# Kernel optimization log

Measured on AMD Instinct MI355X. Metric: run time of the kernel, lower is better.

## Reference

```python
import jax, jax.numpy as jnp
import numpy as np

EPS = 1e-5
NUM_GROUPS = 16


def _deform_conv(x, offset, mask, weight):
    """Modulated deformable conv v2, 3x3, stride 1, pad 1, no bias.
    x: [B,C,H,W], offset: [B,18,H,W] (y,x interleaved per kernel point),
    mask: [B,9,H,W], weight: [O,C,3,3].
    """
    B, C, H, W = x.shape
    O = weight.shape[0]
    K = 9
    off = offset.reshape(B, K, 2, H, W)
    dy, dx = off[:, :, 0], off[:, :, 1]  # [B,K,H,W]
    # base sampling grid: output pixel + kernel tap offset (pad=1 -> taps -1..1)
    ky, kx = jnp.meshgrid(jnp.arange(3), jnp.arange(3), indexing='ij')
    ky = (ky.reshape(K) - 1).astype(x.dtype)
    kx = (kx.reshape(K) - 1).astype(x.dtype)
    iy = jnp.arange(H, dtype=x.dtype)[:, None]
    ix = jnp.arange(W, dtype=x.dtype)[None, :]
    py = iy[None, None] + ky[None, :, None, None] + dy  # [B,K,H,W]
    px = ix[None, None] + kx[None, :, None, None] + dx

    y0 = jnp.floor(py)
    x0 = jnp.floor(px)
    wy = py - y0  # grad flows to offsets via these weights
    wx = px - x0

    xf = x.reshape(B, C, H * W)

    def gather(yc, xc, w):
        # yc,xc,w: [B,K,H,W] float; returns weighted samples [B,C,K,H,W]
        valid = (yc >= 0) & (yc <= H - 1) & (xc >= 0) & (xc <= W - 1)
        yi = jnp.clip(yc, 0, H - 1).astype(jnp.int32)
        xi = jnp.clip(xc, 0, W - 1).astype(jnp.int32)
        idx = (yi * W + xi).reshape(B, K * H * W)
        g = jax.vmap(lambda xb, ib: xb[:, ib])(xf, idx)  # [B,C,K*H*W]
        g = g.reshape(B, C, K, H, W)
        wv = (w * valid.astype(x.dtype))[:, None]  # [B,1,K,H,W]
        return g * wv

    val = gather(y0, x0, (1 - wy) * (1 - wx))
    val = val + gather(y0, x0 + 1, (1 - wy) * wx)
    val = val + gather(y0 + 1, x0, wy * (1 - wx))
    val = val + gather(y0 + 1, x0 + 1, wy * wx)

    val = val * mask[:, None]  # modulation: [B,C,K,H,W] * [B,1,K,H,W]
    w = weight.reshape(O, C, K)
    return jnp.einsum('bckhw,ock->bohw', val, w)


def _group_norm(y, gamma, beta):
    B, O, H, W = y.shape
    g = y.reshape(B, NUM_GROUPS, O // NUM_GROUPS, H, W)
    mean = g.mean(axis=(2, 3, 4), keepdims=True)
    var = ((g - mean) ** 2).mean(axis=(2, 3, 4), keepdims=True)
    g = (g - mean) * jax.lax.rsqrt(var + EPS)
    y = g.reshape(B, O, H, W)
    return y * gamma[None, :, None, None] + beta[None, :, None, None]


def setup_inputs() -> dict:
    key = jax.random.key(0)
    k1, k2, k3, k4 = jax.random.split(key, 4)
    B, C, O, H, W = 8, 256, 256, 64, 64
    x = jax.random.normal(k1, (B, C, H, W), jnp.float32)
    offset = jax.random.normal(k2, (B, 18, H, W), jnp.float32)
    mask = jax.random.uniform(k3, (B, 9, H, W), jnp.float32)
    weight = jax.random.normal(k4, (O, C, 3, 3), jnp.float32) * 0.02
    gamma = jnp.ones((O,), jnp.float32)
    beta = jnp.zeros((O,), jnp.float32)
    return {"x": x, "offset": offset, "mask": mask, "weight": weight,
            "gamma": gamma, "beta": beta}


def reference(x, offset, mask, weight, gamma, beta):
    y = _deform_conv(x, offset, mask, weight)
    return _group_norm(y, gamma, beta)
```

## Files before the change

kernel.cpp:

```cpp
#include <hip/hip_runtime.h>
#include <hip/hip_fp16.h>
#include <math.h>

#define BB 8
#define CC 256
#define OO 256
#define HH 64
#define WW 64
#define KK 9
#define HWSZ 4096
#define CKSZ 2304
#define NG 16
#define OPG 16
#define EPSV 1e-5f

typedef _Float16 f16;
typedef f16 f16x8 __attribute__((ext_vector_type(8)));
typedef float f32x4 __attribute__((ext_vector_type(4)));

#define XH_ELEMS ((size_t)BB*HWSZ*CC)
#define WH_ELEMS ((size_t)OO*CKSZ)
#define CV_ELEMS ((size_t)BB*OO*HWSZ)
#define PSUM_FLOATS ((size_t)512*32)

__device__ __forceinline__ void gload_lds16(const void* g, void* l) {
  __builtin_amdgcn_global_load_lds(
      (const __attribute__((address_space(1))) void*)g,
      (__attribute__((address_space(3))) void*)l, 16, 0, 0);
}

__global__ __launch_bounds__(256) void x_transpose_k(
    const float* __restrict__ x, __half* __restrict__ xh)
{
  int blk = blockIdx.x;
  int b = blk >> 8; int rem = blk & 255;
  int c0 = (rem >> 6) * 64; int hw0 = (rem & 63) * 64;
  __shared__ float st[64][65];
  int t = threadIdx.x;
  #pragma unroll
  for (int i = 0; i < 16; ++i) {
    int idx = t + i*256; int c = idx >> 6, w = idx & 63;
    st[c][w] = x[((size_t)(b*CC + c0 + c))*HWSZ + hw0 + w];
  }
  __syncthreads();
  #pragma unroll
  for (int i = 0; i < 8; ++i) {
    int idx = t + i*256; int r = idx >> 5, cp = idx & 31;
    __half2 v = __floats2half2_rn(st[cp*2][r], st[cp*2+1][r]);
    *(__half2*)&xh[((size_t)(b*HWSZ) + hw0 + r)*CC + c0 + cp*2] = v;
  }
}

__global__ __launch_bounds__(256) void w_reorder_k(
    const float* __restrict__ w, __half* __restrict__ wh)
{
  int i = blockIdx.x*256 + threadIdx.x;
  int o = i / CKSZ; int kp = i - o*CKSZ;
  int kk = kp >> 8, c = kp & 255;
  wh[i] = __float2half(w[o*CKSZ + c*KK + kk]);
}

template<int F16OUT>
__global__ __launch_bounds__(256, 2) void dcn_mfma_k(
    const float* __restrict__ off, const float* __restrict__ msk,
    const __half* __restrict__ xh, const __half* __restrict__ wh,
    float* __restrict__ out32, __half* __restrict__ conv16,
    float* __restrict__ psum)
{
  __shared__ __half sWl[OO*64];
  __shared__ __half sVl[2][64*64];
  __shared__ uint   sTapO[KK][64][4];
  __shared__ __half sTapW[KK][64][4];
  __shared__ float  sRed[4][4][2];

  const int t = threadIdx.x;
  const int b = blockIdx.x & 7;
  const int h = blockIdx.x >> 3;

  const int lane = t & 63, wid = t >> 6;
  const int lr = lane & 15, lh = lane >> 4;
  const int gp = t >> 2, gq = t & 3;

  for (int s = t; s < KK*64; s += 256) {
    int k = s >> 6, p = s & 63;
    float dy = off[(((b*18) + 2*k    )*HH + h)*WW + p];
    float dx = off[(((b*18) + 2*k + 1)*HH + h)*WW + p];
    float m  = msk[(((b*KK) + k)*HH + h)*WW + p];
    float py = (float)(h + (k/3) - 1) + dy;
    float px = (float)(p + (k%3) - 1) + dx;
    float y0f = floorf(py), x0f = floorf(px);
    float wy = py - y0f, wx = px - x0f;
    int y0 = (int)y0f, x0 = (int)x0f;
    #pragma unroll
    for (int tap = 0; tap < 4; ++tap) {
      int yy = y0 + (tap >> 1), xx = x0 + (tap & 1);
      bool v = (yy >= 0) & (yy < HH) & (xx >= 0) & (xx < WW);
      float bw = ((tap >> 1) ? wy : 1.f - wy) * ((tap & 1) ? wx : 1.f - wx);
      float wgt = v ? bw * m : 0.f;
      int cy = min(max(yy, 0), HH-1), cx = min(max(xx, 0), WW-1);
      sTapO[k][p][tap] = (uint)((cy*WW + cx) * (CC*2));
      sTapW[k][p][tap] = __float2half(wgt);
    }
  }
  __syncthreads();

  f32x4 acc[4][4];
  #pragma unroll
  for (int mi = 0; mi < 4; ++mi)
    #pragma unroll
    for (int ni = 0; ni < 4; ++ni) acc[mi][ni] = (f32x4){0.f,0.f,0.f,0.f};

  const char* xbase = (const char*)xh + (size_t)b * (HWSZ*CC*2);

  uint4 tO = *(const uint4*)&sTapO[0][gp][0];
  union { uint2 u; __half hh[4]; } tW;
  tW.u = *(const uint2*)&sTapW[0][gp][0];

  auto gload_sw = [&](int k, int c0) {
    #pragma unroll
    for (int i = 0; i < 8; ++i) {
      int idx = i*256 + t;
      int o = idx >> 3, s = idx & 7;
      const __half* g = wh + (size_t)o*CKSZ + k*256 + c0 + ((s ^ (o & 7)) << 3);
      char* ldsbase = (char*)sWl + (size_t)(i*256 + (t & ~63))*16;
      gload_lds16(g, ldsbase);
    }
  };

  gload_sw(0, 0);
  {
    __half2 w0 = __half2half2(tW.hh[0]), w1 = __half2half2(tW.hh[1]);
    __half2 w2 = __half2half2(tW.hh[2]), w3 = __half2half2(tW.hh[3]);
    #pragma unroll
    for (int oi = 0; oi < 2; ++oi) {
      int oct = gq + oi*4;
      const char* cb = xbase + oct*16;
      uint4 r0 = *(const uint4*)(cb + tO.x);
      uint4 r1 = *(const uint4*)(cb + tO.y);
      uint4 r2 = *(const uint4*)(cb + tO.z);
      uint4 r3 = *(const uint4*)(cb + tO.w);
      const __half2* t0 = (const __half2*)&r0; const __half2* t1 = (const __half2*)&r1;
      const __half2* t2 = (const __half2*)&r2; const __half2* t3 = (const __half2*)&r3;
      __half2 o_[4];
      #pragma unroll
      for (int r = 0; r < 4; ++r)
        o_[r] = __hfma2(w0, t0[r], __hfma2(w1, t1[r],
                __hfma2(w2, t2[r], __hmul2(w3, t3[r]))));
      *(uint4*)&sVl[0][gp*64 + ((oct ^ (gp & 7)) << 3)] = *(uint4*)o_;
    }
  }

  int cur = 0;
  for (int cc = 0; cc < 36; ++cc) {
    const int k = cc >> 2;
    __syncthreads();

    f16x8 areg[2][4];
    #pragma unroll
    for (int ks = 0; ks < 2; ++ks)
      #pragma unroll
      for (int mi = 0; mi < 4; ++mi) {
        int r = wid*64 + mi*16 + lr;
        areg[ks][mi] = *(const f16x8*)&sWl[r*64 + (((ks*4 + lh) ^ (r & 7)) << 3)];
      }
    __syncthreads();

    uint4 ga0, ga1, ga2, ga3, gb0, gb1, gb2, gb3;
    bool pf = (cc + 1 < 36);
    int kn = (cc+1) >> 2, c0n = ((cc+1) & 3) << 6;
    if (pf) {
      gload_sw(kn, c0n);
      if (kn != k) {
        tO = *(const uint4*)&sTapO[kn][gp][0];
        tW.u = *(const uint2*)&sTapW[kn][gp][0];
      }
      const char* cb = xbase + (size_t)(c0n*2) + gq*16;
      ga0 = *(const uint4*)(cb + tO.x);
      ga1 = *(const uint4*)(cb + tO.y);
      ga2 = *(const uint4*)(cb + tO.z);
      ga3 = *(const uint4*)(cb + tO.w);
      gb0 = *(const uint4*)(cb + tO.x + 64);
      gb1 = *(const uint4*)(cb + tO.y + 64);
      gb2 = *(const uint4*)(cb + tO.z + 64);
      gb3 = *(const uint4*)(cb + tO.w + 64);
    }

    #pragma unroll
    for (int ks = 0; ks < 2; ++ks) {
      f16x8 brg[4];
      #pragma unroll
      for (int ni = 0; ni < 4; ++ni) {
        int r = ni*16 + lr;
        brg[ni] = *(const f16x8*)&sVl[cur][r*64 + (((ks*4 + lh) ^ (r & 7)) << 3)];
      }
      #pragma unroll
      for (int mi = 0; mi < 4; ++mi)
        #pragma unroll
        for (int ni = 0; ni < 4; ++ni)
          acc[mi][ni] = __builtin_amdgcn_mfma_f32_16x16x32_f16(
              areg[ks][mi], brg[ni], acc[mi][ni], 0, 0, 0);
    }

    if (pf) {
      __half2 w0 = __half2half2(tW.hh[0]), w1 = __half2half2(tW.hh[1]);
      __half2 w2 = __half2half2(tW.hh[2]), w3 = __half2half2(tW.hh[3]);
      {
        const __half2* t0 = (const __half2*)&ga0; const __half2* t1 = (const __half2*)&ga1;
        const __half2* t2 = (const __half2*)&ga2; const __half2* t3 = (const __half2*)&ga3;
        __half2 o_[4];
        #pragma unroll
        for (int r = 0; r < 4; ++r)
          o_[r] = __hfma2(w0, t0[r], __hfma2(w1, t1[r],
                  __hfma2(w2, t2[r], __hmul2(w3, t3[r]))));
        *(uint4*)&sVl[cur ^ 1][gp*64 + ((gq ^ (gp & 7)) << 3)] = *(uint4*)o_;
      }
      {
        const __half2* t0 = (const __half2*)&gb0; const __half2* t1 = (const __half2*)&gb1;
        const __half2* t2 = (const __half2*)&gb2; const __half2* t3 = (const __half2*)&gb3;
        __half2 o_[4];
        #pragma unroll
        for (int r = 0; r < 4; ++r)
          o_[r] = __hfma2(w0, t0[r], __hfma2(w1, t1[r],
                  __hfma2(w2, t2[r], __hmul2(w3, t3[r]))));
        *(uint4*)&sVl[cur ^ 1][gp*64 + (((gq + 4) ^ (gp & 7)) << 3)] = *(uint4*)o_;
      }
      cur ^= 1;
    }
  }

  #pragma unroll
  for (int mi = 0; mi < 4; ++mi) {
    #pragma unroll
    for (int ni = 0; ni < 4; ++ni) {
      int ob = wid*64 + mi*16 + lh*4;
      int pp = ni*16 + lr;
      #pragma unroll
      for (int j = 0; j < 4; ++j) {
        size_t idx = ((size_t)(b*OO + ob + j))*HWSZ + h*WW + pp;
        if (F16OUT) conv16[idx] = __float2half(acc[mi][ni][j]);
        else        out32[idx] = acc[mi][ni][j];
      }
    }
  }

  if (F16OUT) {
    #pragma unroll
    for (int mi = 0; mi < 4; ++mi) {
      float s1 = 0.f, s2 = 0.f;
      #pragma unroll
      for (int ni = 0; ni < 4; ++ni)
        #pragma unroll
        for (int j = 0; j < 4; ++j) {
          float v = acc[mi][ni][j];
          s1 += v; s2 += v*v;
        }
      #pragma unroll
      for (int d = 32; d > 0; d >>= 1) {
        s1 += __shfl_xor(s1, d);
        s2 += __shfl_xor(s2, d);
      }
      if (lane == 0) { sRed[wid][mi][0] = s1; sRed[wid][mi][1] = s2; }
    }
    __syncthreads();
    if (t < 16) {
      psum[(size_t)blockIdx.x*32 + t*2]     = sRed[t >> 2][t & 3][0];
      psum[(size_t)blockIdx.x*32 + t*2 + 1] = sRed[t >> 2][t & 3][1];
    }
  }
}

__global__ __launch_bounds__(256) void gn_norm2_k(
    const __half* __restrict__ conv16, const float* __restrict__ psum,
    const float* __restrict__ gamma, const float* __restrict__ beta,
    float* __restrict__ out)
{
  int bid = blockIdx.x;
  int bo = bid >> 1;
  int b = bo >> 8, o = bo & 255;
  int g = o >> 4;
  float s1 = 0.f, s2 = 0.f;
  for (int hbl = 0; hbl < 64; ++hbl) {
    s1 += psum[(size_t)(hbl*8 + b)*32 + g*2];
    s2 += psum[(size_t)(hbl*8 + b)*32 + g*2 + 1];
  }
  const float invN = 1.f / (float)(OPG*HWSZ);
  float mean = s1 * invN;
  float var  = s2 * invN - mean*mean;
  float inv = rsqrtf(var + EPSV);
  float sc = gamma[o]*inv;
  float sh = beta[o] - mean*sc;

  size_t e0 = ((size_t)(b*OO + o))*HWSZ + (size_t)(bid & 1)*2048
            + (size_t)threadIdx.x*8;
  uint4 u = *(const uint4*)(conv16 + e0);
  const __half2* hh = (const __half2*)&u;
  float r[8];
  #pragma unroll
  for (int j = 0; j < 4; ++j) {
    float2 f = __half22float2(hh[j]);
    r[2*j] = f.x; r[2*j+1] = f.y;
  }
  *(float4*)&out[e0]     = make_float4(r[0]*sc+sh, r[1]*sc+sh, r[2]*sc+sh, r[3]*sc+sh);
  *(float4*)&out[e0 + 4] = make_float4(r[4]*sc+sh, r[5]*sc+sh, r[6]*sc+sh, r[7]*sc+sh);
}

__global__ __launch_bounds__(1024) void gn_stats_k(
    const float* __restrict__ out, float* __restrict__ stats)
{
  int bg = blockIdx.x;
  const float4* p = (const float4*)(out + (size_t)bg*OPG*HWSZ);
  const int n4 = OPG*HWSZ/4;
  float s1 = 0.f, s2 = 0.f;
  for (int i = threadIdx.x; i < n4; i += 1024) {
    float4 v = p[i];
    s1 += v.x + v.y + v.z + v.w;
    s2 += v.x*v.x + v.y*v.y + v.z*v.z + v.w*v.w;
  }
  #pragma unroll
  for (int o2 = 32; o2 > 0; o2 >>= 1) {
    s1 += __shfl_down(s1, o2);
    s2 += __shfl_down(s2, o2);
  }
  __shared__ float r1[16], r2[16];
  int wd = threadIdx.x >> 6, lane = threadIdx.x & 63;
  if (lane == 0) { r1[wd] = s1; r2[wd] = s2; }
  __syncthreads();
  if (threadIdx.x == 0) {
    float t1 = 0.f, t2 = 0.f;
    #pragma unroll
    for (int i = 0; i < 16; i++) { t1 += r1[i]; t2 += r2[i]; }
    const float invN = 1.f / (float)(OPG*HWSZ);
    float mean = t1 * invN;
    float var  = t2 * invN - mean*mean;
    stats[bg*2]   = mean;
    stats[bg*2+1] = var;
  }
}

__global__ __launch_bounds__(256) void gn_norm_k(
    float* __restrict__ out, const float* __restrict__ stats,
    const float* __restrict__ gamma, const float* __restrict__ beta)
{
  size_t i = (size_t)blockIdx.x*256 + threadIdx.x;
  const size_t n4 = (size_t)BB*OO*HWSZ/4;
  if (i >= n4) return;
  size_t base = i*4;
  int bo = (int)(base / HWSZ);
  int b = bo / OO, o = bo - b*OO;
  int g = o >> 4;
  float mean = stats[(b*NG+g)*2], var = stats[(b*NG+g)*2+1];
  float inv = rsqrtf(var + EPSV);
  float sc = gamma[o]*inv;
  float sh = beta[o] - mean*sc;
  float4 v = *(float4*)&out[base];
  v.x = v.x*sc + sh; v.y = v.y*sc + sh;
  v.z = v.z*sc + sh; v.w = v.w*sc + sh;
  *(float4*)&out[base] = v;
}

extern "C" void kernel_launch(void* const* d_in, const int* in_sizes, int n_in,
                              void* d_out, int out_size, void* d_ws, size_t ws_size,
                              hipStream_t stream) {
  const float* x      = (const float*)d_in[0];
  const float* offset = (const float*)d_in[1];
  const float* mask   = (const float*)d_in[2];
  const float* weight = (const float*)d_in[3];
  const float* gamma  = (const float*)d_in[4];
  const float* beta   = (const float*)d_in[5];
  float* out = (float*)d_out;

  __half* xh   = (__half*)d_ws;
  __half* wh   = xh + XH_ELEMS;
  __half* cv   = wh + WH_ELEMS;
  float* psum  = (float*)(cv + CV_ELEMS);

  const size_t need = (XH_ELEMS + WH_ELEMS + CV_ELEMS)*2 + PSUM_FLOATS*4 + 1024;

  x_transpose_k<<<BB*4*64, 256, 0, stream>>>(x, xh);
  w_reorder_k<<<(int)(WH_ELEMS/256), 256, 0, stream>>>(weight, wh);

  if (ws_size >= need) {
    dcn_mfma_k<1><<<512, 256, 0, stream>>>(offset, mask, xh, wh,
                                           (float*)nullptr, cv, psum);
    gn_norm2_k<<<4096, 256, 0, stream>>>(cv, psum, gamma, beta, out);
  } else {
    float* stats = (float*)(wh + WH_ELEMS);
    dcn_mfma_k<0><<<512, 256, 0, stream>>>(offset, mask, xh, wh,
                                           out, (__half*)nullptr, (float*)nullptr);
    gn_stats_k<<<BB*NG, 1024, 0, stream>>>(out, stats);
    gn_norm_k<<<(int)((size_t)BB*OO*HWSZ/4 + 255)/256, 256, 0, stream>>>(
        out, stats, gamma, beta);
  }
}
```

Baseline: 93.41 us.

## Pre-swizzle weights into MFMA fragment order and load A operands directly from global

The weight reorder kernel now writes fp16 weights in the exact per-lane MFMA A-fragment order, so the main kernel loads A registers straight from global memory (coalesced 16-byte loads) instead of staging a 32KB weight tile through LDS. This removes the LDS weight buffer, one of the two barriers per iteration, and the async global-to-LDS copies. Tap offsets and weights are packed into one 32-bit word per tap, and launch bounds go up to 3 blocks per CU to use the freed LDS. The trade-off is that each wave reloads weight fragments from L2/global every iteration, adding latency that LDS staging used to hide.

```diff
diff --git a/kernel.cpp b/kernel.cpp
--- a/kernel.cpp
+++ b/kernel.cpp
@@ -19,15 +19,9 @@
 typedef float f32x4 __attribute__((ext_vector_type(4)));
 
 #define XH_ELEMS ((size_t)BB*HWSZ*CC)
-#define WH_ELEMS ((size_t)OO*CKSZ)
+#define WF_ELEMS ((size_t)OO*CKSZ)
 #define CV_ELEMS ((size_t)BB*OO*HWSZ)
 #define PSUM_FLOATS ((size_t)512*32)
-
-__device__ __forceinline__ void gload_lds16(const void* g, void* l) {
-  __builtin_amdgcn_global_load_lds(
-      (const __attribute__((address_space(1))) void*)g,
-      (__attribute__((address_space(3))) void*)l, 16, 0, 0);
-}
 
 __global__ __launch_bounds__(256) void x_transpose_k(
     const float* __restrict__ x, __half* __restrict__ xh)
@@ -51,26 +45,27 @@
   }
 }
 
-__global__ __launch_bounds__(256) void w_reorder_k(
-    const float* __restrict__ w, __half* __restrict__ wh)
+__global__ __launch_bounds__(256) void w_frag_k(
+    const float* __restrict__ w, __half* __restrict__ wf)
 {
   int i = blockIdx.x*256 + threadIdx.x;
-  int o = i / CKSZ; int kp = i - o*CKSZ;
-  int kk = kp >> 8, c = kp & 255;
-  wh[i] = __float2half(w[o*CKSZ + c*KK + kk]);
+  int e = i & 7, lane = (i >> 3) & 63, mi = (i >> 9) & 3;
+  int ks = (i >> 11) & 1, wid = (i >> 12) & 3, cc = i >> 14;
+  int k = cc >> 2, c0i = cc & 3;
+  int o = wid*64 + mi*16 + (lane & 15);
+  int c = c0i*64 + ks*32 + (lane >> 4)*8 + e;
+  wf[i] = __float2half(w[(o*CC + c)*KK + k]);
 }
 
 template<int F16OUT>
-__global__ __launch_bounds__(256, 2) void dcn_mfma_k(
+__global__ __launch_bounds__(256, 3) void dcn_mfma_k(
     const float* __restrict__ off, const float* __restrict__ msk,
-    const __half* __restrict__ xh, const __half* __restrict__ wh,
+    const __half* __restrict__ xh, const __half* __restrict__ wf,
     float* __restrict__ out32, __half* __restrict__ conv16,
     float* __restrict__ psum)
 {
-  __shared__ __half sWl[OO*64];
   __shared__ __half sVl[2][64*64];
-  __shared__ uint   sTapO[KK][64][4];
-  __shared__ __half sTapW[KK][64][4];
+  __shared__ uint   sTapP[KK][64][4];
   __shared__ float  sRed[4][4][2];
 
   const int t = threadIdx.x;
@@ -98,8 +93,9 @@
       float bw = ((tap >> 1) ? wy : 1.f - wy) * ((tap & 1) ? wx : 1.f - wx);
       float wgt = v ? bw * m : 0.f;
       int cy = min(max(yy, 0), HH-1), cx = min(max(xx, 0), WW-1);
-      sTapO[k][p][tap] = (uint)((cy*WW + cx) * (CC*2));
-      sTapW[k][p][tap] = __float2half(wgt);
+      uint idx = (uint)(cy*WW + cx);
+      sTapP[k][p][tap] = (idx << 16)
+                       | (uint)__half_as_ushort(__float2half(wgt));
     }
   }
   __syncthreads();
@@ -112,77 +108,75 @@
 
   const char* xbase = (const char*)xh + (size_t)b * (HWSZ*CC*2);
 
-  uint4 tO = *(const uint4*)&sTapO[0][gp][0];
-  union { uint2 u; __half hh[4]; } tW;
-  tW.u = *(const uint2*)&sTapW[0][gp][0];
-
-  auto gload_sw = [&](int k, int c0) {
-    #pragma unroll
-    for (int i = 0; i < 8; ++i) {
-      int idx = i*256 + t;
-      int o = idx >> 3, s = idx & 7;
-      const __half* g = wh + (size_t)o*CKSZ + k*256 + c0 + ((s ^ (o & 7)) << 3);
-      char* ldsbase = (char*)sWl + (size_t)(i*256 + (t & ~63))*16;
-      gload_lds16(g, ldsbase);
-    }
+  uint toff[4]; __half2 twv[4];
+  #pragma unroll
+  for (int i = 0; i < 4; ++i) {
+    uint tp = sTapP[0][gp][i];
+    toff[i] = (tp >> 16) << 9;
+    twv[i]  = __half2half2(__ushort_as_half((unsigned short)(tp & 0xFFFFu)));
+  }
+  int tk = 0;
+
+  auto combine_write = [&](uint4 r0, uint4 r1, uint4 r2, uint4 r3,
+                           int oct, __half* dst) {
+    const __half2* t0 = (const __half2*)&r0; const __half2* t1 = (const __half2*)&r1;
+    const __half2* t2 = (const __half2*)&r2; const __half2* t3 = (const __half2*)&r3;
+    __half2 o_[4];
+    #pragma unroll
+    for (int r = 0; r < 4; ++r)
+      o_[r] = __hfma2(twv[0], t0[r], __hfma2(twv[1], t1[r],
+              __hfma2(twv[2], t2[r], __hmul2(twv[3], t3[r]))));
+    *(uint4*)&dst[gp*64 + ((oct ^ (gp & 7)) << 3)] = *(uint4*)o_;
   };
 
-  gload_sw(0, 0);
   {
-    __half2 w0 = __half2half2(tW.hh[0]), w1 = __half2half2(tW.hh[1]);
-    __half2 w2 = __half2half2(tW.hh[2]), w3 = __half2half2(tW.hh[3]);
-    #pragma unroll
-    for (int oi = 0; oi < 2; ++oi) {
-      int oct = gq + oi*4;
-      const char* cb = xbase + oct*16;
-      uint4 r0 = *(const uint4*)(cb + tO.x);
-      uint4 r1 = *(const uint4*)(cb + tO.y);
-      uint4 r2 = *(const uint4*)(cb + tO.z);
-      uint4 r3 = *(const uint4*)(cb + tO.w);
-      const __half2* t0 = (const __half2*)&r0; const __half2* t1 = (const __half2*)&r1;
-      const __half2* t2 = (const __half2*)&r2; const __half2* t3 = (const __half2*)&r3;
-      __half2 o_[4];
-      #pragma unroll
-      for (int r = 0; r < 4; ++r)
-        o_[r] = __hfma2(w0, t0[r], __hfma2(w1, t1[r],
-                __hfma2(w2, t2[r], __hmul2(w3, t3[r]))));
-      *(uint4*)&sVl[0][gp*64 + ((oct ^ (gp & 7)) << 3)] = *(uint4*)o_;
-    }
+    const char* cb = xbase + gq*16;
+    uint4 a0 = *(const uint4*)(cb + toff[0]);
+    uint4 a1 = *(const uint4*)(cb + toff[1]);
+    uint4 a2 = *(const uint4*)(cb + toff[2]);
+    uint4 a3 = *(const uint4*)(cb + toff[3]);
+    uint4 b0 = *(const uint4*)(cb + toff[0] + 64);
+    uint4 b1 = *(const uint4*)(cb + toff[1] + 64);
+    uint4 b2 = *(const uint4*)(cb + toff[2] + 64);
+    uint4 b3 = *(const uint4*)(cb + toff[3] + 64);
+    combine_write(a0, a1, a2, a3, gq,     sVl[0]);
+    combine_write(b0, b1, b2, b3, gq + 4, sVl[0]);
   }
 
   int cur = 0;
   for (int cc = 0; cc < 36; ++cc) {
-    const int k = cc >> 2;
     __syncthreads();
 
+    const __half* wfp = wf + (size_t)(cc*4 + wid)*4096 + lane*8;
     f16x8 areg[2][4];
     #pragma unroll
     for (int ks = 0; ks < 2; ++ks)
       #pragma unroll
-      for (int mi = 0; mi < 4; ++mi) {
-        int r = wid*64 + mi*16 + lr;
-        areg[ks][mi] = *(const f16x8*)&sWl[r*64 + (((ks*4 + lh) ^ (r & 7)) << 3)];
-      }
-    __syncthreads();
-
-    uint4 ga0, ga1, ga2, ga3, gb0, gb1, gb2, gb3;
+      for (int mi = 0; mi < 4; ++mi)
+        areg[ks][mi] = *(const f16x8*)(wfp + (ks*4 + mi)*512);
+
     bool pf = (cc + 1 < 36);
     int kn = (cc+1) >> 2, c0n = ((cc+1) & 3) << 6;
+    uint4 ga0, ga1, ga2, ga3, gb0, gb1, gb2, gb3;
     if (pf) {
-      gload_sw(kn, c0n);
-      if (kn != k) {
-        tO = *(const uint4*)&sTapO[kn][gp][0];
-        tW.u = *(const uint2*)&sTapW[kn][gp][0];
+      if (kn != tk) {
+        #pragma unroll
+        for (int i = 0; i < 4; ++i) {
+          uint tp = sTapP[kn][gp][i];
+          toff[i] = (tp >> 16) << 9;
+          twv[i]  = __half2half2(__ushort_as_half((unsigned short)(tp & 0xFFFFu)));
+        }
+        tk = kn;
       }
       const char* cb = xbase + (size_t)(c0n*2) + gq*16;
-      ga0 = *(const uint4*)(cb + tO.x);
-      ga1 = *(const uint4*)(cb + tO.y);
-      ga2 = *(const uint4*)(cb + tO.z);
-      ga3 = *(const uint4*)(cb + tO.w);
-      gb0 = *(const uint4*)(cb + tO.x + 64);
-      gb1 = *(const uint4*)(cb + tO.y + 64);
-      gb2 = *(const uint4*)(cb + tO.z + 64);
-      gb3 = *(const uint4*)(cb + tO.w + 64);
+      ga0 = *(const uint4*)(cb + toff[0]);
+      ga1 = *(const uint4*)(cb + toff[1]);
+      ga2 = *(const uint4*)(cb + toff[2]);
+      ga3 = *(const uint4*)(cb + toff[3]);
+      gb0 = *(const uint4*)(cb + toff[0] + 64);
+      gb1 = *(const uint4*)(cb + toff[1] + 64);
+      gb2 = *(const uint4*)(cb + toff[2] + 64);
+      gb3 = *(const uint4*)(cb + toff[3] + 64);
     }
 
     #pragma unroll
@@ -202,28 +196,8 @@
     }
 
     if (pf) {
-      __half2 w0 = __half2half2(tW.hh[0]), w1 = __half2half2(tW.hh[1]);
-      __half2 w2 = __half2half2(tW.hh[2]), w3 = __half2half2(tW.hh[3]);
-      {
-        const __half2* t0 = (const __half2*)&ga0; const __half2* t1 = (const __half2*)&ga1;
-        const __half2* t2 = (const __half2*)&ga2; const __half2* t3 = (const __half2*)&ga3;
-        __half2 o_[4];
-        #pragma unroll
-        for (int r = 0; r < 4; ++r)
-          o_[r] = __hfma2(w0, t0[r], __hfma2(w1, t1[r],
-                  __hfma2(w2, t2[r], __hmul2(w3, t3[r]))));
-        *(uint4*)&sVl[cur ^ 1][gp*64 + ((gq ^ (gp & 7)) << 3)] = *(uint4*)o_;
-      }
-      {
-        const __half2* t0 = (const __half2*)&gb0; const __half2* t1 = (const __half2*)&gb1;
-        const __half2* t2 = (const __half2*)&gb2; const __half2* t3 = (const __half2*)&gb3;
-        __half2 o_[4];
-        #pragma unroll
-        for (int r = 0; r < 4; ++r)
-          o_[r] = __hfma2(w0, t0[r], __hfma2(w1, t1[r],
-                  __hfma2(w2, t2[r], __hmul2(w3, t3[r]))));
-        *(uint4*)&sVl[cur ^ 1][gp*64 + (((gq + 4) ^ (gp & 7)) << 3)] = *(uint4*)o_;
-      }
+      combine_write(ga0, ga1, ga2, ga3, gq,     sVl[cur ^ 1]);
+      combine_write(gb0, gb1, gb2, gb3, gq + 4, sVl[cur ^ 1]);
       cur ^= 1;
     }
   }
@@ -370,22 +344,22 @@
   float* out = (float*)d_out;
 
   __half* xh   = (__half*)d_ws;
-  __half* wh   = xh + XH_ELEMS;
-  __half* cv   = wh + WH_ELEMS;
+  __half* wf   = xh + XH_ELEMS;
+  __half* cv   = wf + WF_ELEMS;
   float* psum  = (float*)(cv + CV_ELEMS);
 
-  const size_t need = (XH_ELEMS + WH_ELEMS + CV_ELEMS)*2 + PSUM_FLOATS*4 + 1024;
+  const size_t need = (XH_ELEMS + WF_ELEMS + CV_ELEMS)*2 + PSUM_FLOATS*4 + 1024;
 
   x_transpose_k<<<BB*4*64, 256, 0, stream>>>(x, xh);
-  w_reorder_k<<<(int)(WH_ELEMS/256), 256, 0, stream>>>(weight, wh);
+  w_frag_k<<<(int)(WF_ELEMS/256), 256, 0, stream>>>(weight, wf);
 
   if (ws_size >= need) {
-    dcn_mfma_k<1><<<512, 256, 0, stream>>>(offset, mask, xh, wh,
+    dcn_mfma_k<1><<<512, 256, 0, stream>>>(offset, mask, xh, wf,
                                            (float*)nullptr, cv, psum);
     gn_norm2_k<<<4096, 256, 0, stream>>>(cv, psum, gamma, beta, out);
   } else {
-    float* stats = (float*)(wh + WH_ELEMS);
-    dcn_mfma_k<0><<<512, 256, 0, stream>>>(offset, mask, xh, wh,
+    float* stats = (float*)(wf + WF_ELEMS);
+    dcn_mfma_k<0><<<512, 256, 0, stream>>>(offset, mask, xh, wf,
                                            out, (__half*)nullptr, (float*)nullptr);
     gn_stats_k<<<BB*NG, 1024, 0, stream>>>(out, stats);
     gn_norm_k<<<(int)((size_t)BB*OO*HWSZ/4 + 255)/256, 256, 0, stream>>>(
```

After: 89.66 us. -4.0%, faster.
